# Performance work log

Measured on AMD Instinct MI355X. Metric: run time of the kernel, lower is better.

Reference implementation:

```python
import jax, jax.numpy as jnp
import numpy as np

N_NODES = 100000; N_RELS = 100; EMB = 128; HID = 768; LAYERS = 12
CW = 3; HEADS = 12; DH = HID // HEADS; FF = 4 * HID
B = 256; S = 128


def _statics():
    # Sliding-window mask from build_mask(): rows with offset <= S-L get the
    # submask [0]*2cw + [-inf] + [0]*2cw at [offset:offset+L]; remaining rows
    # are all -inf (we neutralize those rows to avoid NaN; their attn output
    # is zeroed, see VALID).
    Lw = 4 * CW + 1
    r = np.arange(S)[:, None]; c = np.arange(S)[None, :]
    valid = np.arange(S) <= S - Lw
    inwin = (c >= r) & (c < r + Lw) & (c != r + 2 * CW) & valid[:, None]
    addmask = np.where(inwin, 0.0, -np.inf).astype(np.float32)
    addmask = np.where(valid[:, None], addmask, 0.0)
    ri, ci = np.nonzero(inwin)  # selection indices for pos_dist[:, mask]
    # sinusoidal positional encoding (S, HID)
    pos = np.arange(S)[:, None].astype(np.float32)
    div = np.exp(-np.log(10000.0) * np.arange(0, HID, 2) / HID)
    pe = np.zeros((S, HID), np.float32)
    pe[:, 0::2] = np.sin(pos * div); pe[:, 1::2] = np.cos(pos * div)
    return (jnp.asarray(addmask), jnp.asarray(valid), jnp.asarray(ri),
            jnp.asarray(ci), jnp.asarray(pe))

ADDMASK, VALID, RI, CI, PE = _statics()


def _ln(x, g, b, eps=1e-5):
    m = jnp.mean(x, -1, keepdims=True)
    v = jnp.mean((x - m) ** 2, -1, keepdims=True)
    return (x - m) * jax.lax.rsqrt(v + eps) * g + b


def setup_inputs() -> dict:
    key = jax.random.key(0)
    ks = iter(jax.random.split(key, 40))
    nrm = lambda shp, s=0.02: jax.random.normal(next(ks), shp, jnp.float32) * s
    V = N_NODES + N_RELS
    d = {}
    d['seq'] = jax.random.randint(next(ks), (B, S), 0, V, jnp.int32)
    d['neg_idx'] = jax.random.randint(next(ks), (B, S), 0, N_NODES, jnp.int32)
    d['embed_W'] = nrm((V, EMB), 1.0)
    d['embed_g'] = jnp.ones((EMB,)); d['embed_b'] = jnp.zeros((EMB,))
    d['proj_W'] = nrm((EMB, HID)); d['proj_b'] = jnp.zeros((HID,))
    d['qkv_W'] = nrm((LAYERS, HID, 3 * HID)); d['qkv_b'] = jnp.zeros((LAYERS, 3 * HID))
    d['ao_W'] = nrm((LAYERS, HID, HID)); d['ao_b'] = jnp.zeros((LAYERS, HID))
    d['ln1_g'] = jnp.ones((LAYERS, HID)); d['ln1_b'] = jnp.zeros((LAYERS, HID))
    d['ff1_W'] = nrm((LAYERS, HID, FF)); d['ff1_b'] = jnp.zeros((LAYERS, FF))
    d['ff2_W'] = nrm((LAYERS, FF, HID)); d['ff2_b'] = jnp.zeros((LAYERS, HID))
    d['ln2_g'] = jnp.ones((LAYERS, HID)); d['ln2_b'] = jnp.zeros((LAYERS, HID))
    d['head_W'] = nrm((HID, EMB)); d['head_b'] = jnp.zeros((EMB,))
    d['head_g'] = jnp.ones((EMB,)); d['head_beta'] = jnp.zeros((EMB,))
    d['oemb_W'] = nrm((V, EMB), 1.0)
    d['oemb_g'] = jnp.ones((EMB,)); d['oemb_b'] = jnp.zeros((EMB,))
    return d


def reference(seq, neg_idx, embed_W, embed_g, embed_b, proj_W, proj_b,
              qkv_W, qkv_b, ao_W, ao_b, ln1_g, ln1_b, ff1_W, ff1_b,
              ff2_W, ff2_b, ln2_g, ln2_b, head_W, head_b, head_g, head_beta,
              oemb_W, oemb_g, oemb_b):
    b, s = seq.shape
    z = _ln(embed_W[seq], embed_g, embed_b)                 # (B,S,E)
    x = jax.nn.gelu(z @ proj_W + proj_b, approximate=False)  # (B,S,H)
    x = x + PE[None, :, :]
    vrow = VALID.astype(x.dtype)[None, None, :, None]

    def layer(x, p):
        qkv = x @ p['qw'] + p['qb']
        q, k, v = jnp.split(qkv, 3, axis=-1)
        q = q.reshape(b, s, HEADS, DH); k = k.reshape(b, s, HEADS, DH)
        v = v.reshape(b, s, HEADS, DH)
        scores = jnp.einsum('bihd,bjhd->bhij', q, k) / np.sqrt(DH)
        attn = jax.nn.softmax(scores + ADDMASK, axis=-1) * vrow
        ctx = jnp.einsum('bhij,bjhd->bihd', attn, v).reshape(b, s, HID)
        x = _ln(x + ctx @ p['aw'] + p['ab'], p['g1'], p['b1'])
        h = jax.nn.gelu(x @ p['f1w'] + p['f1b'], approximate=False)
        x = _ln(x + h @ p['f2w'] + p['f2b'], p['g2'], p['b2'])
        return x, None

    params = {'qw': qkv_W, 'qb': qkv_b, 'aw': ao_W, 'ab': ao_b,
              'g1': ln1_g, 'b1': ln1_b, 'f1w': ff1_W, 'f1b': ff1_b,
              'f2w': ff2_W, 'f2b': ff2_b, 'g2': ln2_g, 'b2': ln2_b}
    x, _ = jax.lax.scan(layer, x, params)

    preds = _ln(x @ head_W + head_b, head_g, head_beta)     # (B,S,E)
    out_z = _ln(oemb_W[seq], oemb_g, oemb_b)                # (B,S,E)
    pos_dist = jnp.einsum('bie,bje->bij', out_z, preds)     # (B,S,S)
    pos = pos_dist[:, RI, CI].reshape(-1, 2 * CW).mean(-1)
    neg_e = _ln(oemb_W[neg_idx], oemb_g, oemb_b)
    neg_dist = jnp.einsum('bie,bje->bij', out_z, neg_e)
    neg = neg_dist[:, RI, CI].reshape(-1, 2 * CW).mean(-1)
    # BCEWithLogitsLoss: labels 1 for pos, 0 for neg, mean reduction
    n = pos.shape[0] + neg.shape[0]
    loss = (jnp.sum(jax.nn.softplus(-pos)) + jnp.sum(jax.nn.softplus(neg))) / n
    return loss
```

## Files before the change

### kernel.cpp

```cpp
#include <hip/hip_runtime.h>
#include <hip/hip_bf16.h>

typedef __hip_bfloat16 bf16;
typedef __bf16 bf16x8 __attribute__((ext_vector_type(8)));
typedef float f32x4 __attribute__((ext_vector_type(4)));

#define B_      256
#define S_      128
#define HID_    768
#define EMB_    128
#define FF_     3072
#define LAYERS_ 12
#define HEADS_  12
#define DH_     64
#define M_TOK   (B_ * S_)

__device__ inline float b2f(bf16 v) { return __bfloat162float(v); }
__device__ inline bf16  f2b(float v) { return __float2bfloat16(v); }

__device__ inline float wave_sum(float v) {
#pragma unroll
  for (int o = 32; o > 0; o >>= 1) v += __shfl_xor(v, o, 64);
  return v;
}

__device__ inline float gelu_exact(float x) {
  return 0.5f * x * (1.0f + erff(x * 0.70710678118654752f));
}

__device__ inline void glds16(const bf16* g, bf16* l) {
  __builtin_amdgcn_global_load_lds(
      (const __attribute__((address_space(1))) void*)g,
      (__attribute__((address_space(3))) void*)l, 16, 0, 0);
}

__global__ __launch_bounds__(256)
void gemm_bt(const bf16* __restrict__ A, const bf16* __restrict__ Bt,
             const float* __restrict__ bias, bf16* __restrict__ C,
             int M, int N, int K, int mode)
{
  __shared__ __align__(16) bf16 As[128 * 32];
  __shared__ __align__(16) bf16 Bs[128 * 32];
  const int tid  = threadIdx.x;
  const int wave = tid >> 6, lane = tid & 63;
  const int m0 = blockIdx.y * 128, n0 = blockIdx.x * 128;

  const int ar = lane >> 2;
  const int ac = (lane & 3) * 8;
  const int c0 = wave * 2;
  const bf16* ga0 = A  + (size_t)(m0 + c0 * 16      + ar) * K + ac;
  const bf16* ga1 = A  + (size_t)(m0 + (c0+1) * 16  + ar) * K + ac;
  const bf16* gb0 = Bt + (size_t)(n0 + c0 * 16      + ar) * K + ac;
  const bf16* gb1 = Bt + (size_t)(n0 + (c0+1) * 16  + ar) * K + ac;
  bf16* lA0 = As + c0 * 512;       bf16* lA1 = As + (c0 + 1) * 512;
  bf16* lB0 = Bs + c0 * 512;       bf16* lB1 = Bs + (c0 + 1) * 512;

  const int lr = lane & 15;
  const int lk = (lane >> 4) * 8;
  const int rm = (wave >> 1) * 64;
  const int rn = (wave & 1) * 64;

  const f32x4 zacc = {0.f, 0.f, 0.f, 0.f};
  f32x4 acc[4][4];
#pragma unroll
  for (int i = 0; i < 4; i++)
#pragma unroll
    for (int j = 0; j < 4; j++) acc[i][j] = zacc;

  for (int k0 = 0; k0 < K; k0 += 32) {
    glds16(ga0 + k0, lA0);
    glds16(ga1 + k0, lA1);
    glds16(gb0 + k0, lB0);
    glds16(gb1 + k0, lB1);
    __syncthreads();
    bf16x8 af[4], bfr[4];
#pragma unroll
    for (int i = 0; i < 4; i++) af[i]  = *(const bf16x8*)&As[(rm + i * 16 + lr) * 32 + lk];
#pragma unroll
    for (int j = 0; j < 4; j++) bfr[j] = *(const bf16x8*)&Bs[(rn + j * 16 + lr) * 32 + lk];
#pragma unroll
    for (int i = 0; i < 4; i++)
#pragma unroll
      for (int j = 0; j < 4; j++)
        acc[i][j] = __builtin_amdgcn_mfma_f32_16x16x32_bf16(af[i], bfr[j], acc[i][j], 0, 0, 0);
    __syncthreads();
  }

  const int er = (lane >> 4) * 4;
  const int ec = lane & 15;
#pragma unroll
  for (int i = 0; i < 4; i++) {
    const int row = m0 + rm + i * 16 + er;
#pragma unroll
    for (int j = 0; j < 4; j++) {
      const int col = n0 + rn + j * 16 + ec;
      const float bv = bias[col];
#pragma unroll
      for (int r = 0; r < 4; r++) {
        float v = acc[i][j][r] + bv;
        if (mode >= 1) v = gelu_exact(v);
        if (mode == 2) {
          const int srow = (row + r) & (S_ - 1);
          const int i2 = col & ~1;
          const float div = expf(-9.210340371976184f * (float)i2 * (1.0f / (float)HID_));
          const float ang = (float)srow * div;
          v += (col & 1) ? cosf(ang) : sinf(ang);
        }
        C[(size_t)(row + r) * N + col] = f2b(v);
      }
    }
  }
}

__global__ __launch_bounds__(256)
void convtrans(const float* __restrict__ src, bf16* __restrict__ dst, int K, int N)
{
  __shared__ bf16 t[32][33];
  const int n0 = blockIdx.x * 32, k0 = blockIdx.y * 32;
  const int tx = threadIdx.x, ty = threadIdx.y;
#pragma unroll
  for (int i = 0; i < 4; i++)
    t[ty + i * 8][tx] = f2b(src[(size_t)(k0 + ty + i * 8) * N + n0 + tx]);
  __syncthreads();
#pragma unroll
  for (int i = 0; i < 4; i++)
    dst[(size_t)(n0 + ty + i * 8) * K + k0 + tx] = t[tx][ty + i * 8];
}

__global__ __launch_bounds__(128)
void attn_kernel(const bf16* __restrict__ qkv, bf16* __restrict__ ctx)
{
  const int bh = blockIdx.x;
  const int b = bh / HEADS_, h = bh % HEADS_;
  __shared__ __align__(16) bf16 qs[S_ * DH_];
  __shared__ __align__(16) bf16 ks[S_ * DH_];
  __shared__ __align__(16) bf16 vs[S_ * DH_];
  const int tid = threadIdx.x;
  const bf16* base = qkv + (size_t)b * S_ * (3 * HID_) + h * DH_;
  for (int it = 0; it < 8; ++it) {
    const int s = it * 16 + (tid >> 3);
    const int seg = (tid & 7) * 8;
    const size_t go = (size_t)s * (3 * HID_) + seg;
    *(uint4*)&qs[s * DH_ + seg] = *(const uint4*)&base[go];
    *(uint4*)&ks[s * DH_ + seg] = *(const uint4*)&base[go + HID_];
    *(uint4*)&vs[s * DH_ + seg] = *(const uint4*)&base[go + 2 * HID_];
  }
  __syncthreads();
  const int i = tid;
  bf16* out = ctx + (size_t)(b * S_ + i) * HID_ + h * DH_;
  if (i < 116) {
    float p[13];
    float mx = -1e30f;
    for (int jj = 0; jj < 13; jj++) {
      if (jj == 6) { p[jj] = 0.f; continue; }
      float d = 0.f;
#pragma unroll
      for (int dd = 0; dd < DH_; dd++) d += b2f(qs[i * DH_ + dd]) * b2f(ks[(i + jj) * DH_ + dd]);
      p[jj] = d * 0.125f;
      mx = fmaxf(mx, p[jj]);
    }
    float l = 0.f;
    for (int jj = 0; jj < 13; jj++) {
      if (jj == 6) { p[jj] = 0.f; continue; }
      p[jj] = expf(p[jj] - mx);
      l += p[jj];
    }
    const float inv = 1.f / l;
    float o[DH_];
#pragma unroll
    for (int dd = 0; dd < DH_; dd++) o[dd] = 0.f;
    for (int jj = 0; jj < 13; jj++) {
      if (jj == 6) continue;
      const float pj = p[jj] * inv;
#pragma unroll
      for (int dd = 0; dd < DH_; dd++) o[dd] += pj * b2f(vs[(i + jj) * DH_ + dd]);
    }
#pragma unroll
    for (int dd = 0; dd < DH_; dd++) out[dd] = f2b(o[dd]);
  } else {
#pragma unroll
    for (int dd = 0; dd < DH_; dd++) out[dd] = f2b(0.f);
  }
}

__global__ __launch_bounds__(256)
void add_ln_kernel(const bf16* __restrict__ x, const bf16* __restrict__ y,
                   const float* __restrict__ g, const float* __restrict__ bta,
                   bf16* __restrict__ out)
{
  const int r = blockIdx.x, tid = threadIdx.x;
  const size_t base = (size_t)r * HID_;
  float v[3];
#pragma unroll
  for (int e = 0; e < 3; e++) {
    const int idx = tid + e * 256;
    v[e] = b2f(x[base + idx]) + b2f(y[base + idx]);
  }
  float s  = v[0] + v[1] + v[2];
  float ss = v[0] * v[0] + v[1] * v[1] + v[2] * v[2];
  s = wave_sum(s);
  ss = wave_sum(ss);
  __shared__ float red[8];
  const int wave = tid >> 6, lane = tid & 63;
  if (lane == 0) { red[wave] = s; red[4 + wave] = ss; }
  __syncthreads();
  s  = red[0] + red[1] + red[2] + red[3];
  ss = red[4] + red[5] + red[6] + red[7];
  const float mean = s * (1.f / (float)HID_);
  const float var  = ss * (1.f / (float)HID_) - mean * mean;
  const float rs = rsqrtf(var + 1e-5f);
#pragma unroll
  for (int e = 0; e < 3; e++) {
    const int idx = tid + e * 256;
    out[base + idx] = f2b((v[e] - mean) * rs * g[idx] + bta[idx]);
  }
}

__global__ __launch_bounds__(256)
void gather_ln128(const int* __restrict__ idx, const float* __restrict__ W,
                  const float* __restrict__ g, const float* __restrict__ bta,
                  bf16* __restrict__ out)
{
  const int token = blockIdx.x * 4 + (threadIdx.x >> 6);
  const int lane = threadIdx.x & 63;
  const int row = idx[token];
  const float* src = W + (size_t)row * 128;
  const float a = src[lane], c = src[lane + 64];
  const float s  = wave_sum(a + c);
  const float ss = wave_sum(a * a + c * c);
  const float mean = s * (1.f / 128.f);
  const float var  = ss * (1.f / 128.f) - mean * mean;
  const float rs = rsqrtf(var + 1e-5f);
  bf16* o = out + (size_t)token * 128;
  o[lane]      = f2b((a - mean) * rs * g[lane] + bta[lane]);
  o[lane + 64] = f2b((c - mean) * rs * g[lane + 64] + bta[lane + 64]);
}

__global__ __launch_bounds__(256)
void ln128_bf16(const bf16* __restrict__ in, const float* __restrict__ g,
                const float* __restrict__ bta, bf16* __restrict__ out)
{
  const int token = blockIdx.x * 4 + (threadIdx.x >> 6);
  const int lane = threadIdx.x & 63;
  const bf16* src = in + (size_t)token * 128;
  const float a = b2f(src[lane]), c = b2f(src[lane + 64]);
  const float s  = wave_sum(a + c);
  const float ss = wave_sum(a * a + c * c);
  const float mean = s * (1.f / 128.f);
  const float var  = ss * (1.f / 128.f) - mean * mean;
  const float rs = rsqrtf(var + 1e-5f);
  bf16* o = out + (size_t)token * 128;
  o[lane]      = f2b((a - mean) * rs * g[lane] + bta[lane]);
  o[lane + 64] = f2b((c - mean) * rs * g[lane + 64] + bta[lane + 64]);
}

__global__ __launch_bounds__(256)
void loss_kernel(const bf16* __restrict__ out_z, const bf16* __restrict__ preds,
                 const bf16* __restrict__ neg_e, float* __restrict__ out)
{
  const int b = blockIdx.x;
  const int which = blockIdx.y;
  __shared__ __align__(16) bf16 zo[128 * 128];
  __shared__ __align__(16) bf16 mt[128 * 128];
  const bf16* msrc = which ? neg_e : preds;
  const uint4* gz = (const uint4*)(out_z + (size_t)b * 16384);
  const uint4* gm = (const uint4*)(msrc + (size_t)b * 16384);
  for (int it = threadIdx.x; it < 2048; it += 256) {
    ((uint4*)zo)[it] = gz[it];
    ((uint4*)mt)[it] = gm[it];
  }
  __syncthreads();
  float local = 0.f;
  for (int it = threadIdx.x; it < 232; it += 256) {
    const int i = it >> 1;
    const int sub = it & 1;
    const int c0 = i + (sub ? 7 : 0);
    const bf16* zr = &zo[i * 128];
    float accv = 0.f;
    for (int jj = 0; jj < 6; jj++) {
      const bf16* mr = &mt[(c0 + jj) * 128];
      float d = 0.f;
#pragma unroll
      for (int dd = 0; dd < 128; dd++) d += b2f(zr[dd]) * b2f(mr[dd]);
      accv += d;
    }
    const float mean = accv * (1.f / 6.f);
    const float xin = which ? mean : -mean;
    local += fmaxf(xin, 0.f) + log1pf(expf(-fabsf(xin)));
  }
  local = wave_sum(local);
  if ((threadIdx.x & 63) == 0)
    atomicAdd(out, local * (1.f / 118784.f));
}

__global__ void zero_kernel(float* p) { p[0] = 0.f; }

extern "C" void kernel_launch(void* const* d_in, const int* in_sizes, int n_in,
                              void* d_out, int out_size, void* d_ws, size_t ws_size,
                              hipStream_t stream)
{
  (void)in_sizes; (void)n_in; (void)out_size; (void)ws_size;
  const int*   seq     = (const int*)  d_in[0];
  const int*   neg_idx = (const int*)  d_in[1];
  const float* embed_W = (const float*)d_in[2];
  const float* embed_g = (const float*)d_in[3];
  const float* embed_b = (const float*)d_in[4];
  const float* proj_W  = (const float*)d_in[5];
  const float* proj_b  = (const float*)d_in[6];
  const float* qkv_W   = (const float*)d_in[7];
  const float* qkv_b   = (const float*)d_in[8];
  const float* ao_W    = (const float*)d_in[9];
  const float* ao_b    = (const float*)d_in[10];
  const float* ln1_g   = (const float*)d_in[11];
  const float* ln1_b   = (const float*)d_in[12];
  const float* ff1_W   = (const float*)d_in[13];
  const float* ff1_b   = (const float*)d_in[14];
  const float* ff2_W   = (const float*)d_in[15];
  const float* ff2_b   = (const float*)d_in[16];
  const float* ln2_g   = (const float*)d_in[17];
  const float* ln2_b   = (const float*)d_in[18];
  const float* head_W  = (const float*)d_in[19];
  const float* head_b  = (const float*)d_in[20];
  const float* head_g  = (const float*)d_in[21];
  const float* head_bt = (const float*)d_in[22];
  const float* oemb_W  = (const float*)d_in[23];
  const float* oemb_g  = (const float*)d_in[24];
  const float* oemb_b  = (const float*)d_in[25];
  float* out = (float*)d_out;

  char* ws = (char*)d_ws;
  size_t off = 0;
  auto alloc = [&](size_t bytes) -> char* {
    char* p = ws + off;
    off += (bytes + 255) & ~(size_t)255;
    return p;
  };
  bf16* wt_qkv  = (bf16*)alloc((size_t)2304 * 768 * 2);
  bf16* wt_ao   = (bf16*)alloc((size_t)768 * 768 * 2);
  bf16* wt_ff1  = (bf16*)alloc((size_t)3072 * 768 * 2);
  bf16* wt_ff2  = (bf16*)alloc((size_t)768 * 3072 * 2);
  bf16* wt_proj = (bf16*)alloc((size_t)768 * 128 * 2);
  bf16* wt_head = (bf16*)alloc((size_t)128 * 768 * 2);
  bf16* zbuf    = (bf16*)alloc((size_t)M_TOK * 128 * 2);
  bf16* x       = (bf16*)alloc((size_t)M_TOK * 768 * 2);
  bf16* big     = (bf16*)alloc((size_t)M_TOK * 3072 * 2);
  bf16* ctx     = (bf16*)alloc((size_t)M_TOK * 768 * 2);
  bf16* ybuf    = (bf16*)alloc((size_t)M_TOK * 768 * 2);
  bf16* p0      = (bf16*)alloc((size_t)M_TOK * 128 * 2);
  bf16* preds   = (bf16*)alloc((size_t)M_TOK * 128 * 2);
  bf16* outz    = (bf16*)alloc((size_t)M_TOK * 128 * 2);
  bf16* nege    = (bf16*)alloc((size_t)M_TOK * 128 * 2);

  const dim3 tb(32, 8);

  convtrans<<<dim3(768 / 32, 128 / 32), tb, 0, stream>>>(proj_W, wt_proj, 128, 768);
  convtrans<<<dim3(128 / 32, 768 / 32), tb, 0, stream>>>(head_W, wt_head, 768, 128);

  gather_ln128<<<M_TOK / 4, 256, 0, stream>>>(seq, embed_W, embed_g, embed_b, zbuf);
  gemm_bt<<<dim3(768 / 128, M_TOK / 128), 256, 0, stream>>>(zbuf, wt_proj, proj_b, x,
                                                            M_TOK, 768, 128, 2);

  for (int l = 0; l < LAYERS_; ++l) {
    convtrans<<<dim3(2304 / 32, 768 / 32), tb, 0, stream>>>(qkv_W + (size_t)l * 768 * 2304, wt_qkv, 768, 2304);
    convtrans<<<dim3(768 / 32, 768 / 32), tb, 0, stream>>>(ao_W + (size_t)l * 768 * 768, wt_ao, 768, 768);
    convtrans<<<dim3(3072 / 32, 768 / 32), tb, 0, stream>>>(ff1_W + (size_t)l * 768 * 3072, wt_ff1, 768, 3072);
    convtrans<<<dim3(768 / 32, 3072 / 32), tb, 0, stream>>>(ff2_W + (size_t)l * 3072 * 768, wt_ff2, 3072, 768);

    gemm_bt<<<dim3(2304 / 128, M_TOK / 128), 256, 0, stream>>>(x, wt_qkv, qkv_b + l * 2304, big,
                                                               M_TOK, 2304, 768, 0);
    attn_kernel<<<B_ * HEADS_, 128, 0, stream>>>(big, ctx);
    gemm_bt<<<dim3(768 / 128, M_TOK / 128), 256, 0, stream>>>(ctx, wt_ao, ao_b + l * 768, ybuf,
                                                              M_TOK, 768, 768, 0);
    add_ln_kernel<<<M_TOK, 256, 0, stream>>>(x, ybuf, ln1_g + l * 768, ln1_b + l * 768, x);
    gemm_bt<<<dim3(3072 / 128, M_TOK / 128), 256, 0, stream>>>(x, wt_ff1, ff1_b + l * 3072, big,
                                                               M_TOK, 3072, 768, 1);
    gemm_bt<<<dim3(768 / 128, M_TOK / 128), 256, 0, stream>>>(big, wt_ff2, ff2_b + l * 768, ybuf,
                                                              M_TOK, 768, 3072, 0);
    add_ln_kernel<<<M_TOK, 256, 0, stream>>>(x, ybuf, ln2_g + l * 768, ln2_b + l * 768, x);
  }

  gemm_bt<<<dim3(1, M_TOK / 128), 256, 0, stream>>>(x, wt_head, head_b, p0, M_TOK, 128, 768, 0);
  ln128_bf16<<<M_TOK / 4, 256, 0, stream>>>(p0, head_g, head_bt, preds);
  gather_ln128<<<M_TOK / 4, 256, 0, stream>>>(seq, oemb_W, oemb_g, oemb_b, outz);
  gather_ln128<<<M_TOK / 4, 256, 0, stream>>>(neg_idx, oemb_W, oemb_g, oemb_b, nege);
  zero_kernel<<<1, 1, 0, stream>>>(out);
  loss_kernel<<<dim3(B_, 2), 256, 0, stream>>>(outz, preds, nege, out);
}
```

Measured before the change: 12.01 ms.

## Rework GEMM tiling to K=64 with fragment-ordered LDS, vectorize attention and layernorm

```diff
diff --git a/kernel.cpp b/kernel.cpp
--- a/kernel.cpp
+++ b/kernel.cpp
@@ -3,6 +3,7 @@
 
 typedef __hip_bfloat16 bf16;
 typedef __bf16 bf16x8 __attribute__((ext_vector_type(8)));
+typedef __bf16 bf16x4 __attribute__((ext_vector_type(4)));
 typedef float f32x4 __attribute__((ext_vector_type(4)));
 
 #define B_      256
@@ -39,26 +40,30 @@
              const float* __restrict__ bias, bf16* __restrict__ C,
              int M, int N, int K, int mode)
 {
-  __shared__ __align__(16) bf16 As[128 * 32];
-  __shared__ __align__(16) bf16 Bs[128 * 32];
+  __shared__ __align__(16) bf16 As[128 * 64];
+  __shared__ __align__(16) bf16 Bs[128 * 64];
   const int tid  = threadIdx.x;
   const int wave = tid >> 6, lane = tid & 63;
   const int m0 = blockIdx.y * 128, n0 = blockIdx.x * 128;
-
-  const int ar = lane >> 2;
-  const int ac = (lane & 3) * 8;
-  const int c0 = wave * 2;
-  const bf16* ga0 = A  + (size_t)(m0 + c0 * 16      + ar) * K + ac;
-  const bf16* ga1 = A  + (size_t)(m0 + (c0+1) * 16  + ar) * K + ac;
-  const bf16* gb0 = Bt + (size_t)(n0 + c0 * 16      + ar) * K + ac;
-  const bf16* gb1 = Bt + (size_t)(n0 + (c0+1) * 16  + ar) * K + ac;
-  bf16* lA0 = As + c0 * 512;       bf16* lA1 = As + (c0 + 1) * 512;
-  bf16* lB0 = Bs + c0 * 512;       bf16* lB1 = Bs + (c0 + 1) * 512;
-
-  const int lr = lane & 15;
-  const int lk = (lane >> 4) * 8;
+  const int lr = lane & 15, lkg = lane >> 4;
+
+  const bf16* gA[4]; const bf16* gB[4];
+  bf16 *lA[4], *lB[4];
+#pragma unroll
+  for (int c = 0; c < 4; c++) {
+    const int s = wave * 4 + c;
+    const int row = (s >> 1) * 16 + lr;
+    const int col = (s & 1) * 32 + lkg * 8;
+    gA[c] = A  + (size_t)(m0 + row) * K + col;
+    gB[c] = Bt + (size_t)(n0 + row) * K + col;
+    lA[c] = As + s * 512;
+    lB[c] = Bs + s * 512;
+  }
+
   const int rm = (wave >> 1) * 64;
   const int rn = (wave & 1) * 64;
+  const int aSlab = (wave >> 1) * 4;
+  const int bSlab = (wave & 1) * 4;
 
   const f32x4 zacc = {0.f, 0.f, 0.f, 0.f};
   f32x4 acc[4][4];
@@ -67,56 +72,65 @@
 #pragma unroll
     for (int j = 0; j < 4; j++) acc[i][j] = zacc;
 
-  for (int k0 = 0; k0 < K; k0 += 32) {
-    glds16(ga0 + k0, lA0);
-    glds16(ga1 + k0, lA1);
-    glds16(gb0 + k0, lB0);
-    glds16(gb1 + k0, lB1);
+  for (int k0 = 0; k0 < K; k0 += 64) {
+#pragma unroll
+    for (int c = 0; c < 4; c++) glds16(gA[c] + k0, lA[c]);
+#pragma unroll
+    for (int c = 0; c < 4; c++) glds16(gB[c] + k0, lB[c]);
     __syncthreads();
-    bf16x8 af[4], bfr[4];
-#pragma unroll
-    for (int i = 0; i < 4; i++) af[i]  = *(const bf16x8*)&As[(rm + i * 16 + lr) * 32 + lk];
-#pragma unroll
-    for (int j = 0; j < 4; j++) bfr[j] = *(const bf16x8*)&Bs[(rn + j * 16 + lr) * 32 + lk];
-#pragma unroll
-    for (int i = 0; i < 4; i++)
+#pragma unroll
+    for (int kk = 0; kk < 2; kk++) {
+      bf16x8 af[4], bfr[4];
+#pragma unroll
+      for (int i = 0; i < 4; i++)
+        af[i] = *(const bf16x8*)&As[((aSlab + i) * 2 + kk) * 512 + lane * 8];
 #pragma unroll
       for (int j = 0; j < 4; j++)
-        acc[i][j] = __builtin_amdgcn_mfma_f32_16x16x32_bf16(af[i], bfr[j], acc[i][j], 0, 0, 0);
+        bfr[j] = *(const bf16x8*)&Bs[((bSlab + j) * 2 + kk) * 512 + lane * 8];
+#pragma unroll
+      for (int i = 0; i < 4; i++)
+#pragma unroll
+        for (int j = 0; j < 4; j++)
+          acc[i][j] = __builtin_amdgcn_mfma_f32_16x16x32_bf16(bfr[j], af[i], acc[i][j], 0, 0, 0);
+    }
     __syncthreads();
   }
 
-  const int er = (lane >> 4) * 4;
-  const int ec = lane & 15;
 #pragma unroll
   for (int i = 0; i < 4; i++) {
-    const int row = m0 + rm + i * 16 + er;
+    const int m = m0 + rm + i * 16 + lr;
+    bf16* crow = C + (size_t)m * N;
 #pragma unroll
     for (int j = 0; j < 4; j++) {
-      const int col = n0 + rn + j * 16 + ec;
-      const float bv = bias[col];
+      const int nb = n0 + rn + j * 16 + (lkg << 2);
+      const float4 bv = *(const float4*)&bias[nb];
+      const float* bvp = (const float*)&bv;
+      bf16 h[4];
 #pragma unroll
       for (int r = 0; r < 4; r++) {
-        float v = acc[i][j][r] + bv;
-        if (mode >= 1) v = gelu_exact(v);
+        float t = acc[i][j][r] + bvp[r];
+        if (mode == 1) t = gelu_exact(t);
         if (mode == 2) {
-          const int srow = (row + r) & (S_ - 1);
+          t = gelu_exact(t);
+          const int col = nb + r;
+          const int srow = m & (S_ - 1);
           const int i2 = col & ~1;
           const float div = expf(-9.210340371976184f * (float)i2 * (1.0f / (float)HID_));
           const float ang = (float)srow * div;
-          v += (col & 1) ? cosf(ang) : sinf(ang);
+          t += (col & 1) ? cosf(ang) : sinf(ang);
         }
-        C[(size_t)(row + r) * N + col] = f2b(v);
+        h[r] = f2b(t);
       }
-    }
-  }
-}
-
-__global__ __launch_bounds__(256)
-void convtrans(const float* __restrict__ src, bf16* __restrict__ dst, int K, int N)
+      *(uint2*)&crow[nb] = *(const uint2*)h;
+    }
+  }
+}
+
+__device__ inline void convtrans_tile(const float* __restrict__ src, bf16* __restrict__ dst,
+                                      int K, int N, int bx, int by)
 {
   __shared__ bf16 t[32][33];
-  const int n0 = blockIdx.x * 32, k0 = blockIdx.y * 32;
+  const int n0 = bx * 32, k0 = by * 32;
   const int tx = threadIdx.x, ty = threadIdx.y;
 #pragma unroll
   for (int i = 0; i < 4; i++)
@@ -127,59 +141,109 @@
     dst[(size_t)(n0 + ty + i * 8) * K + k0 + tx] = t[tx][ty + i * 8];
 }
 
+__global__ __launch_bounds__(256)
+void convtrans(const float* __restrict__ src, bf16* __restrict__ dst, int K, int N)
+{
+  convtrans_tile(src, dst, K, N, blockIdx.x, blockIdx.y);
+}
+
+__global__ __launch_bounds__(256)
+void convtrans4(const float* __restrict__ qkvW, const float* __restrict__ aoW,
+                const float* __restrict__ ff1W, const float* __restrict__ ff2W,
+                bf16* __restrict__ dqkv, bf16* __restrict__ dao,
+                bf16* __restrict__ dff1, bf16* __restrict__ dff2)
+{
+  const int bid = blockIdx.x;
+  if (bid < 1728) {
+    convtrans_tile(qkvW, dqkv, 768, 2304, bid % 72, bid / 72);
+  } else if (bid < 2304) {
+    const int t = bid - 1728;
+    convtrans_tile(aoW, dao, 768, 768, t % 24, t / 24);
+  } else if (bid < 4608) {
+    const int t = bid - 2304;
+    convtrans_tile(ff1W, dff1, 768, 3072, t % 96, t / 96);
+  } else {
+    const int t = bid - 4608;
+    convtrans_tile(ff2W, dff2, 3072, 768, t % 24, t / 24);
+  }
+}
+
 __global__ __launch_bounds__(128)
 void attn_kernel(const bf16* __restrict__ qkv, bf16* __restrict__ ctx)
 {
   const int bh = blockIdx.x;
   const int b = bh / HEADS_, h = bh % HEADS_;
-  __shared__ __align__(16) bf16 qs[S_ * DH_];
-  __shared__ __align__(16) bf16 ks[S_ * DH_];
-  __shared__ __align__(16) bf16 vs[S_ * DH_];
+  __shared__ __align__(16) bf16 qs[8 * 128 * 8];
+  __shared__ __align__(16) bf16 ks[8 * 128 * 8];
+  __shared__ __align__(16) bf16 vs[8 * 128 * 8];
   const int tid = threadIdx.x;
   const bf16* base = qkv + (size_t)b * S_ * (3 * HID_) + h * DH_;
-  for (int it = 0; it < 8; ++it) {
-    const int s = it * 16 + (tid >> 3);
-    const int seg = (tid & 7) * 8;
-    const size_t go = (size_t)s * (3 * HID_) + seg;
-    *(uint4*)&qs[s * DH_ + seg] = *(const uint4*)&base[go];
-    *(uint4*)&ks[s * DH_ + seg] = *(const uint4*)&base[go + HID_];
-    *(uint4*)&vs[s * DH_ + seg] = *(const uint4*)&base[go + 2 * HID_];
+  for (int it = tid; it < 1024; it += 128) {
+    const int s = it & 127, c = it >> 7;
+    const size_t go = (size_t)s * (3 * HID_) + c * 8;
+    *(uint4*)&qs[it * 8] = *(const uint4*)&base[go];
+    *(uint4*)&ks[it * 8] = *(const uint4*)&base[go + HID_];
+    *(uint4*)&vs[it * 8] = *(const uint4*)&base[go + 2 * HID_];
   }
   __syncthreads();
   const int i = tid;
   bf16* out = ctx + (size_t)(b * S_ + i) * HID_ + h * DH_;
   if (i < 116) {
-    float p[13];
+    float d[13];
+#pragma unroll
+    for (int jj = 0; jj < 13; jj++) d[jj] = 0.f;
+#pragma unroll
+    for (int c = 0; c < 8; c++) {
+      const bf16x8 q8 = *(const bf16x8*)&qs[c * 1024 + i * 8];
+#pragma unroll
+      for (int jj = 0; jj < 13; jj++) {
+        if (jj == 6) continue;
+        const bf16x8 k8 = *(const bf16x8*)&ks[c * 1024 + (i + jj) * 8];
+        float s = 0.f;
+#pragma unroll
+        for (int e = 0; e < 8; e++) s += (float)q8[e] * (float)k8[e];
+        d[jj] += s;
+      }
+    }
     float mx = -1e30f;
-    for (int jj = 0; jj < 13; jj++) {
-      if (jj == 6) { p[jj] = 0.f; continue; }
-      float d = 0.f;
-#pragma unroll
-      for (int dd = 0; dd < DH_; dd++) d += b2f(qs[i * DH_ + dd]) * b2f(ks[(i + jj) * DH_ + dd]);
-      p[jj] = d * 0.125f;
-      mx = fmaxf(mx, p[jj]);
-    }
-    float l = 0.f;
-    for (int jj = 0; jj < 13; jj++) {
-      if (jj == 6) { p[jj] = 0.f; continue; }
-      p[jj] = expf(p[jj] - mx);
-      l += p[jj];
-    }
-    const float inv = 1.f / l;
-    float o[DH_];
-#pragma unroll
-    for (int dd = 0; dd < DH_; dd++) o[dd] = 0.f;
+#pragma unroll
     for (int jj = 0; jj < 13; jj++) {
       if (jj == 6) continue;
-      const float pj = p[jj] * inv;
-#pragma unroll
-      for (int dd = 0; dd < DH_; dd++) o[dd] += pj * b2f(vs[(i + jj) * DH_ + dd]);
-    }
-#pragma unroll
-    for (int dd = 0; dd < DH_; dd++) out[dd] = f2b(o[dd]);
+      d[jj] *= 0.125f;
+      mx = fmaxf(mx, d[jj]);
+    }
+    float l = 0.f;
+#pragma unroll
+    for (int jj = 0; jj < 13; jj++) {
+      if (jj == 6) { d[jj] = 0.f; continue; }
+      d[jj] = expf(d[jj] - mx);
+      l += d[jj];
+    }
+    const float inv = 1.f / l;
+#pragma unroll
+    for (int jj = 0; jj < 13; jj++) d[jj] *= inv;
+#pragma unroll
+    for (int c = 0; c < 8; c++) {
+      float o8[8];
+#pragma unroll
+      for (int e = 0; e < 8; e++) o8[e] = 0.f;
+#pragma unroll
+      for (int jj = 0; jj < 13; jj++) {
+        if (jj == 6) continue;
+        const float pj = d[jj];
+        const bf16x8 v8 = *(const bf16x8*)&vs[c * 1024 + (i + jj) * 8];
+#pragma unroll
+        for (int e = 0; e < 8; e++) o8[e] += pj * (float)v8[e];
+      }
+      bf16 hh[8];
+#pragma unroll
+      for (int e = 0; e < 8; e++) hh[e] = f2b(o8[e]);
+      *(uint4*)&out[c * 8] = *(const uint4*)hh;
+    }
   } else {
-#pragma unroll
-    for (int dd = 0; dd < DH_; dd++) out[dd] = f2b(0.f);
+    const uint4 z = {0, 0, 0, 0};
+#pragma unroll
+    for (int c = 0; c < 8; c++) *(uint4*)&out[c * 8] = z;
   }
 }
 
@@ -188,32 +252,38 @@
                    const float* __restrict__ g, const float* __restrict__ bta,
                    bf16* __restrict__ out)
 {
-  const int r = blockIdx.x, tid = threadIdx.x;
-  const size_t base = (size_t)r * HID_;
-  float v[3];
-#pragma unroll
-  for (int e = 0; e < 3; e++) {
-    const int idx = tid + e * 256;
-    v[e] = b2f(x[base + idx]) + b2f(y[base + idx]);
-  }
-  float s  = v[0] + v[1] + v[2];
-  float ss = v[0] * v[0] + v[1] * v[1] + v[2] * v[2];
-  s = wave_sum(s);
-  ss = wave_sum(ss);
-  __shared__ float red[8];
-  const int wave = tid >> 6, lane = tid & 63;
-  if (lane == 0) { red[wave] = s; red[4 + wave] = ss; }
-  __syncthreads();
-  s  = red[0] + red[1] + red[2] + red[3];
-  ss = red[4] + red[5] + red[6] + red[7];
+  const int row  = blockIdx.x * 4 + (threadIdx.x >> 6);
+  const int lane = threadIdx.x & 63;
+  const size_t base = (size_t)row * HID_;
+  const bf16x8 a8 = *(const bf16x8*)&x[base + lane * 8];
+  const bf16x8 b8 = *(const bf16x8*)&y[base + lane * 8];
+  const bf16x4 a4 = *(const bf16x4*)&x[base + 512 + lane * 4];
+  const bf16x4 b4 = *(const bf16x4*)&y[base + 512 + lane * 4];
+  float v[12];
+#pragma unroll
+  for (int e = 0; e < 8; e++) v[e] = (float)a8[e] + (float)b8[e];
+#pragma unroll
+  for (int e = 0; e < 4; e++) v[8 + e] = (float)a4[e] + (float)b4[e];
+  float s = 0.f, ss = 0.f;
+#pragma unroll
+  for (int e = 0; e < 12; e++) { s += v[e]; ss += v[e] * v[e]; }
+  s = wave_sum(s); ss = wave_sum(ss);
   const float mean = s * (1.f / (float)HID_);
   const float var  = ss * (1.f / (float)HID_) - mean * mean;
   const float rs = rsqrtf(var + 1e-5f);
-#pragma unroll
-  for (int e = 0; e < 3; e++) {
-    const int idx = tid + e * 256;
-    out[base + idx] = f2b((v[e] - mean) * rs * g[idx] + bta[idx]);
-  }
+  bf16 h8[8]; bf16 h4[4];
+#pragma unroll
+  for (int e = 0; e < 8; e++) {
+    const int col = lane * 8 + e;
+    h8[e] = f2b((v[e] - mean) * rs * g[col] + bta[col]);
+  }
+#pragma unroll
+  for (int e = 0; e < 4; e++) {
+    const int col = 512 + lane * 4 + e;
+    h4[e] = f2b((v[8 + e] - mean) * rs * g[col] + bta[col]);
+  }
+  *(uint4*)&out[base + lane * 8]       = *(const uint4*)h8;
+  *(uint2*)&out[base + 512 + lane * 4] = *(const uint2*)h4;
 }
 
 __global__ __launch_bounds__(256)
@@ -279,10 +349,15 @@
     float accv = 0.f;
     for (int jj = 0; jj < 6; jj++) {
       const bf16* mr = &mt[(c0 + jj) * 128];
-      float d = 0.f;
-#pragma unroll
-      for (int dd = 0; dd < 128; dd++) d += b2f(zr[dd]) * b2f(mr[dd]);
-      accv += d;
+      float dsum = 0.f;
+#pragma unroll
+      for (int cc = 0; cc < 16; cc++) {
+        const bf16x8 z8 = *(const bf16x8*)&zr[cc * 8];
+        const bf16x8 m8 = *(const bf16x8*)&mr[cc * 8];
+#pragma unroll
+        for (int e = 0; e < 8; e++) dsum += (float)z8[e] * (float)m8[e];
+      }
+      accv += dsum;
     }
     const float mean = accv * (1.f / 6.f);
     const float xin = which ? mean : -mean;
@@ -361,22 +436,22 @@
                                                             M_TOK, 768, 128, 2);
 
   for (int l = 0; l < LAYERS_; ++l) {
-    convtrans<<<dim3(2304 / 32, 768 / 32), tb, 0, stream>>>(qkv_W + (size_t)l * 768 * 2304, wt_qkv, 768, 2304);
-    convtrans<<<dim3(768 / 32, 768 / 32), tb, 0, stream>>>(ao_W + (size_t)l * 768 * 768, wt_ao, 768, 768);
-    convtrans<<<dim3(3072 / 32, 768 / 32), tb, 0, stream>>>(ff1_W + (size_t)l * 768 * 3072, wt_ff1, 768, 3072);
-    convtrans<<<dim3(768 / 32, 3072 / 32), tb, 0, stream>>>(ff2_W + (size_t)l * 3072 * 768, wt_ff2, 3072, 768);
+    convtrans4<<<6912, tb, 0, stream>>>(
+        qkv_W + (size_t)l * 768 * 2304, ao_W + (size_t)l * 768 * 768,
+        ff1_W + (size_t)l * 768 * 3072, ff2_W + (size_t)l * 3072 * 768,
+        wt_qkv, wt_ao, wt_ff1, wt_ff2);
 
     gemm_bt<<<dim3(2304 / 128, M_TOK / 128), 256, 0, stream>>>(x, wt_qkv, qkv_b + l * 2304, big,
                                                                M_TOK, 2304, 768, 0);
     attn_kernel<<<B_ * HEADS_, 128, 0, stream>>>(big, ctx);
     gemm_bt<<<dim3(768 / 128, M_TOK / 128), 256, 0, stream>>>(ctx, wt_ao, ao_b + l * 768, ybuf,
                                                               M_TOK, 768, 768, 0);
-    add_ln_kernel<<<M_TOK, 256, 0, stream>>>(x, ybuf, ln1_g + l * 768, ln1_b + l * 768, x);
+    add_ln_kernel<<<M_TOK / 4, 256, 0, stream>>>(x, ybuf, ln1_g + l * 768, ln1_b + l * 768, x);
     gemm_bt<<<dim3(3072 / 128, M_TOK / 128), 256, 0, stream>>>(x, wt_ff1, ff1_b + l * 3072, big,
                                                                M_TOK, 3072, 768, 1);
     gemm_bt<<<dim3(768 / 128, M_TOK / 128), 256, 0, stream>>>(big, wt_ff2, ff2_b + l * 768, ybuf,
                                                               M_TOK, 768, 3072, 0);
-    add_ln_kernel<<<M_TOK, 256, 0, stream>>>(x, ybuf, ln2_g + l * 768, ln2_b + l * 768, x);
+    add_ln_kernel<<<M_TOK / 4, 256, 0, stream>>>(x, ybuf, ln2_g + l * 768, ln2_b + l * 768, x);
   }
 
   gemm_bt<<<dim3(1, M_TOK / 128), 256, 0, stream>>>(x, wt_head, head_b, p0, M_TOK, 128, 768, 0);
```

After: 15.79 ms. +31.4%, slower.
